# Kernel tuning notes

Measured on AMD Instinct MI355X. Metric: run time of the kernel, lower is better.

## Reference

```python
import jax, jax.numpy as jnp
import numpy as np

B, T, HID = 8, 1024, 1024
N_HEADS, HEAD = 16, HID // 16
MAX_F, BASE = 1024, 10000.0


def _rope_tables():
    inv_freq = 1.0 / (BASE ** (np.arange(0, HEAD, 2, dtype=np.float32) / HEAD))
    t = np.arange(MAX_F, dtype=np.float32)
    freqs = np.einsum('i,j->ij', t, inv_freq)  # (MAX_F, HEAD/2)
    emb = np.concatenate([freqs, freqs], axis=-1)  # (MAX_F, HEAD)
    return jnp.asarray(np.cos(emb)), jnp.asarray(np.sin(emb))


def setup_inputs() -> dict:
    key = jax.random.key(0)
    ks = jax.random.split(key, 6)
    x = jax.random.normal(ks[0], (B, T, HID), dtype=jnp.float32)
    Wq = jax.random.normal(ks[1], (HID, HID), dtype=jnp.float32) * 0.02
    Wk = jax.random.normal(ks[2], (HID, HID), dtype=jnp.float32) * 0.02
    Wv = jax.random.normal(ks[3], (HID, HID), dtype=jnp.float32) * 0.02
    Wo = jax.random.normal(ks[4], (HID, HID), dtype=jnp.float32) * 0.02
    cos, sin = _rope_tables()
    attn_mask = jnp.ones((B, T, T), dtype=jnp.int32)
    timestamp = jax.random.randint(ks[5], (B, T), 0, MAX_F, dtype=jnp.int32)
    return {"x": x, "Wq": Wq, "Wk": Wk, "Wv": Wv, "Wo": Wo,
            "cos": cos, "sin": sin, "attn_mask": attn_mask, "timestamp": timestamp}


def _rotate_half(u):
    u1, u2 = u[..., : HEAD // 2], u[..., HEAD // 2:]
    return jnp.concatenate([-u2, u1], axis=-1)


def reference(x, Wq, Wk, Wv, Wo, cos, sin, attn_mask, timestamp):
    Bx, Tx, _ = x.shape
    # QKV projections (nn.Linear: x @ W.T), reshape to (B, H, T, head)
    def proj(W):
        return (x @ W.T).reshape(Bx, Tx, N_HEADS, HEAD).transpose(0, 2, 1, 3)
    q, k, v = proj(Wq), proj(Wk), proj(Wv)
    # RoPE: gather cos/sin by timestamp, broadcast over heads (unsqueeze dim 1)
    c = cos[timestamp][:, None]  # (B, 1, T, head)
    s = sin[timestamp][:, None]
    q = q * c + _rotate_half(q) * s
    k = k * c + _rotate_half(k) * s
    # Masked SDPA
    scale = 1.0 / jnp.sqrt(jnp.float32(HEAD))
    scores = jnp.einsum('bhqd,bhkd->bhqk', q, k) * scale
    mask = attn_mask[:, None].astype(bool)  # (B, 1, T, T) broadcasts over heads
    scores = jnp.where(mask, scores, jnp.finfo(scores.dtype).min)
    attn = jax.nn.softmax(scores, axis=-1)
    out = jnp.einsum('bhqk,bhkd->bhqd', attn, v)
    out = out.transpose(0, 2, 1, 3).reshape(Bx, Tx, HID)
    return out @ Wo.T
```

## Files before the change

### kernel.cpp

```cpp
#include <hip/hip_runtime.h>
#include <hip/hip_bf16.h>

#define B_   8
#define T_   1024
#define HID_ 1024
#define NH_  16
#define HD_  64
#define K2   2048

typedef __attribute__((ext_vector_type(8))) short bf16x8;
typedef __attribute__((ext_vector_type(4))) float f32x4;

__device__ __forceinline__ void gl_lds16(const void* g, void* l) {
    __builtin_amdgcn_global_load_lds((const __attribute__((address_space(1))) void*)g,
                                     (__attribute__((address_space(3))) void*)l, 16, 0, 0);
}

__device__ __forceinline__ float fast_exp2(float x) {
    return __builtin_amdgcn_exp2f(x);
}

__global__ __launch_bounds__(256) void cast_bf16(const float* __restrict__ X,
                                                 __hip_bfloat16* __restrict__ Y) {
    int gid = blockIdx.x * 256 + threadIdx.x;
    int f = gid << 2;
    float4 xv = *(const float4*)(X + f);
    union { __hip_bfloat16 b[4]; ushort4 u; } p;
    p.b[0] = __float2bfloat16(xv.x);
    p.b[1] = __float2bfloat16(xv.y);
    p.b[2] = __float2bfloat16(xv.z);
    p.b[3] = __float2bfloat16(xv.w);
    *(ushort4*)(Y + f) = p.u;
}

__global__ __launch_bounds__(256) void dup_bf16_w(const float* __restrict__ X,
                                                  __hip_bfloat16* __restrict__ Y) {
    int gid = blockIdx.x * 256 + threadIdx.x;
    int f = gid << 2;
    int m = f >> 10, kk = f & 1023;
    float4 xv = *(const float4*)(X + f);
    union { __hip_bfloat16 b[4]; ushort4 u; } ph;
    ph.b[0] = __float2bfloat16(xv.x);
    ph.b[1] = __float2bfloat16(xv.y);
    ph.b[2] = __float2bfloat16(xv.z);
    ph.b[3] = __float2bfloat16(xv.w);
    size_t base = (size_t)m * K2 + kk;
    *(ushort4*)(Y + base) = ph.u;
    *(ushort4*)(Y + base + 1024) = ph.u;
}

__global__ __launch_bounds__(256) void mask_pack(const int* __restrict__ mask,
                                                 unsigned long long* __restrict__ mbits) {
    int gid = blockIdx.x * 256 + threadIdx.x;
    int wid = gid >> 6;
    int lane = threadIdx.x & 63;
    int m = mask[(size_t)wid * 64 + lane];
    unsigned long long bal = __ballot(m != 0);
    if (lane == 0) mbits[wid] = bal;
}

__global__ __launch_bounds__(256) void mask_dense(const unsigned long long* __restrict__ mbits,
                                                  unsigned int* __restrict__ tdense) {
    int gid = blockIdx.x * 256 + threadIdx.x;
    int e = gid >> 6;
    int lane = threadIdx.x & 63;
    int b = e >> 8, qt = (e >> 4) & 15, kt = e & 15;
    unsigned long long val = mbits[((size_t)(b * T_ + qt * 64 + lane)) * 16 + kt];
    unsigned long long bal = __ballot(val == ~0ull);
    if (lane == 0) tdense[e] = (bal == ~0ull) ? 1u : 0u;
}

template<int MODE, int KD>
__global__ __launch_bounds__(256, 4) void gemm_mfma(const __hip_bfloat16* __restrict__ A,
                                                    const __hip_bfloat16* __restrict__ Wp,
                                                    float* __restrict__ C0,
                                                    __hip_bfloat16* __restrict__ qbf,
                                                    __hip_bfloat16* __restrict__ kbf,
                                                    __hip_bfloat16* __restrict__ vt,
                                                    const float* __restrict__ cost,
                                                    const float* __restrict__ sint,
                                                    const int* __restrict__ ts) {
    __shared__ __hip_bfloat16 As[2][128 * 32];
    __shared__ __hip_bfloat16 Bs[2][128 * 32];
    const int tid = threadIdx.x;
    const int lane = tid & 63;
    const int w = tid >> 6;
    const int wm = w >> 1, wn = w & 1;
    const int m0 = blockIdx.y * 128, n0 = blockIdx.x * 128;
    const int r0 = tid >> 2;
    const int ks = (tid & 3) << 3;
    const int ml = lane & 15;
    const int kg = (lane >> 4) << 3;
    const int q4 = (lane >> 4) << 2;

    f32x4 acc[4][4];
#pragma unroll
    for (int i = 0; i < 4; ++i)
#pragma unroll
        for (int j = 0; j < 4; ++j) acc[i][j] = (f32x4){0.f, 0.f, 0.f, 0.f};

    for (int k0 = 0; k0 < KD; k0 += 64) {
#pragma unroll
        for (int c = 0; c < 2; ++c) {
            const int kc = k0 + c * 32 + ks;
            gl_lds16(A  + (size_t)(m0 + r0)      * KD + kc, &As[c][r0 * 32 + ks]);
            gl_lds16(A  + (size_t)(m0 + 64 + r0) * KD + kc, &As[c][(64 + r0) * 32 + ks]);
            gl_lds16(Wp + (size_t)(n0 + r0)      * KD + kc, &Bs[c][r0 * 32 + ks]);
            gl_lds16(Wp + (size_t)(n0 + 64 + r0) * KD + kc, &Bs[c][(64 + r0) * 32 + ks]);
        }
        __syncthreads();

#pragma unroll
        for (int c = 0; c < 2; ++c) {
            bf16x8 a[4], b[4];
#pragma unroll
            for (int mi = 0; mi < 4; ++mi)
                a[mi] = *(const bf16x8*)(&As[c][(wm * 64 + mi * 16 + ml) * 32 + kg]);
#pragma unroll
            for (int ni = 0; ni < 4; ++ni)
                b[ni] = *(const bf16x8*)(&Bs[c][(wn * 64 + ni * 16 + ml) * 32 + kg]);
#pragma unroll
            for (int mi = 0; mi < 4; ++mi)
#pragma unroll
                for (int ni = 0; ni < 4; ++ni)
                    acc[mi][ni] = __builtin_amdgcn_mfma_f32_16x16x32_bf16(a[mi], b[ni], acc[mi][ni], 0, 0, 0);
        }
        __syncthreads();
    }

    if (MODE == 0) {
#pragma unroll
        for (int mi = 0; mi < 4; ++mi)
#pragma unroll
            for (int ni = 0; ni < 4; ++ni) {
                int n = n0 + wn * 64 + ni * 16 + ml;
#pragma unroll
                for (int r = 0; r < 4; ++r) {
                    int m = m0 + wm * 64 + mi * 16 + q4 + r;
                    C0[(size_t)m * 1024 + n] = acc[mi][ni][r];
                }
            }
    } else {
        const int nB = n0 + wn * 64;
        const int sel = nB >> 10;
        const int h = (nB & 1023) >> 6;
        if (sel < 2) {
            __hip_bfloat16* dst = sel ? kbf : qbf;
#pragma unroll
            for (int mi = 0; mi < 4; ++mi) {
#pragma unroll
                for (int r = 0; r < 4; ++r) {
                    int m = m0 + wm * 64 + mi * 16 + q4 + r;
                    int tsv = ts[m];
                    int bb = m >> 10, t = m & 1023;
                    size_t rowoff = ((size_t)(bb * NH_ + h) * T_ + t) * HD_;
#pragma unroll
                    for (int ni = 0; ni < 4; ++ni) {
                        int d = ni * 16 + ml;
                        float c = cost[tsv * HD_ + d];
                        float s = sint[tsv * HD_ + d];
                        float u  = acc[mi][ni][r];
                        float up = acc[mi][ni ^ 2][r];
                        float o = (ni < 2) ? (u * c - up * s) : (u * c + up * s);
                        dst[rowoff + d] = __float2bfloat16(o);
                    }
                }
            }
        } else {
#pragma unroll
            for (int mi = 0; mi < 4; ++mi)
#pragma unroll
                for (int r = 0; r < 4; ++r) {
                    int m = m0 + wm * 64 + mi * 16 + q4 + r;
                    int bb = m >> 10, t = m & 1023;
#pragma unroll
                    for (int ni = 0; ni < 4; ++ni) {
                        int d = ni * 16 + ml;
                        vt[((size_t)(bb * NH_ + h) * HD_ + d) * T_ + t] =
                            __float2bfloat16(acc[mi][ni][r]);
                    }
                }
        }
    }
}

__global__ __launch_bounds__(256, 4) void flash_mfma(const __hip_bfloat16* __restrict__ qg,
                                                     const __hip_bfloat16* __restrict__ kg_,
                                                     const __hip_bfloat16* __restrict__ vtg,
                                                     const unsigned long long* __restrict__ mbits,
                                                     const unsigned int* __restrict__ tdense,
                                                     __hip_bfloat16* __restrict__ xs) {
    __shared__ __hip_bfloat16 Ks[2][64 * 64];
    __shared__ __hip_bfloat16 Vt[2][64 * 64];
    __shared__ __hip_bfloat16 Ps[4][16 * 64];
    const int id = blockIdx.x;
    const int qt = (id >> 3) & 15;
    const int hb = ((id >> 7) << 3) | (id & 7);
    const int h = hb & 15, b = hb >> 4;
    const int tid = threadIdx.x;
    const int lane = tid & 63;
    const int w = tid >> 6;
    const int ml = lane & 15;
    const int g4 = lane >> 4;
    const int kg8 = g4 << 3;
    const int q4 = g4 << 2;
    const int q0 = qt * 64;
    const size_t bh_off = (size_t)(b * NH_ + h) * T_ * HD_;
    const __hip_bfloat16* qb = qg + bh_off;
    const __hip_bfloat16* kb = kg_ + bh_off;
    const __hip_bfloat16* vtb = vtg + bh_off;
    const float SCL = 0.125f * 1.44269504f;

    const int srow = lane >> 3;
    const int sg8 = ((lane & 7) ^ srow) << 3;
    const int sx = ((g4 ^ (ml & 7)) << 4);
    const int pswz = (ml & 7) << 4;

    bf16x8 qf0 = *(const bf16x8*)(qb + (size_t)(q0 + w * 16 + ml) * HD_ + kg8);
    bf16x8 qf1 = *(const bf16x8*)(qb + (size_t)(q0 + w * 16 + ml) * HD_ + 32 + kg8);

    f32x4 acc_o[4];
    float lsum = 0.f;
#pragma unroll
    for (int i = 0; i < 4; ++i) acc_o[i] = (f32x4){0.f, 0.f, 0.f, 0.f};
    char* psw = (char*)&Ps[w][0];

#pragma unroll
    for (int p = 0; p < 2; ++p) {
        const int rbase = p * 32 + w * 8;
        gl_lds16(kb  + (size_t)(rbase + srow) * HD_ + sg8, &Ks[0][rbase * 64]);
        gl_lds16(vtb + (size_t)(rbase + srow) * T_  + sg8, &Vt[0][rbase * 64]);
    }

    for (int kt = 0; kt < 16; ++kt) {
        const int cur = kt & 1;
        __syncthreads();
        if (kt < 15) {
            const int k0n = (kt + 1) * 64;
            const int nb = cur ^ 1;
#pragma unroll
            for (int p = 0; p < 2; ++p) {
                const int rbase = p * 32 + w * 8;
                gl_lds16(kb  + (size_t)(k0n + rbase + srow) * HD_ + sg8, &Ks[nb][rbase * 64]);
                gl_lds16(vtb + (size_t)(rbase + srow) * T_ + k0n + sg8, &Vt[nb][rbase * 64]);
            }
        }

        f32x4 sacc[4];
#pragma unroll
        for (int ni = 0; ni < 4; ++ni) sacc[ni] = (f32x4){0.f, 0.f, 0.f, 0.f};
        const char* ksb = (const char*)&Ks[cur][0];
#pragma unroll
        for (int ni = 0; ni < 4; ++ni) {
            const char* rp = ksb + (ni * 16 + ml) * 128;
            bf16x8 kf0 = *(const bf16x8*)(rp + sx);
            bf16x8 kf1 = *(const bf16x8*)(rp + (sx ^ 64));
            sacc[ni] = __builtin_amdgcn_mfma_f32_16x16x32_bf16(kf0, qf0, sacc[ni], 0, 0, 0);
            sacc[ni] = __builtin_amdgcn_mfma_f32_16x16x32_bf16(kf1, qf1, sacc[ni], 0, 0, 0);
        }

        if (tdense[(b * 16 + qt) * 16 + kt]) {
#pragma unroll
            for (int ni = 0; ni < 4; ++ni) {
                float pv[4];
#pragma unroll
                for (int r = 0; r < 4; ++r) pv[r] = fast_exp2(sacc[ni][r] * SCL);
                lsum += (pv[0] + pv[1]) + (pv[2] + pv[3]);
                union { __hip_bfloat16 bb[4]; unsigned long long u8; } pk;
                pk.bb[0] = __float2bfloat16(pv[0]);
                pk.bb[1] = __float2bfloat16(pv[1]);
                pk.bb[2] = __float2bfloat16(pv[2]);
                pk.bb[3] = __float2bfloat16(pv[3]);
                *(unsigned long long*)(psw + ml * 128 + ((ni * 32 + g4 * 8) ^ pswz)) = pk.u8;
            }
        } else {
            unsigned long long mb =
                mbits[((size_t)(b * T_ + q0 + w * 16 + ml)) * 16 + kt];
#pragma unroll
            for (int ni = 0; ni < 4; ++ni) {
                float pv[4];
#pragma unroll
                for (int r = 0; r < 4; ++r) {
                    int kv = ni * 16 + q4 + r;
                    pv[r] = ((mb >> kv) & 1ull) ? fast_exp2(sacc[ni][r] * SCL) : 0.f;
                }
                lsum += (pv[0] + pv[1]) + (pv[2] + pv[3]);
                union { __hip_bfloat16 bb[4]; unsigned long long u8; } pk;
                pk.bb[0] = __float2bfloat16(pv[0]);
                pk.bb[1] = __float2bfloat16(pv[1]);
                pk.bb[2] = __float2bfloat16(pv[2]);
                pk.bb[3] = __float2bfloat16(pv[3]);
                *(unsigned long long*)(psw + ml * 128 + ((ni * 32 + g4 * 8) ^ pswz)) = pk.u8;
            }
        }

        bf16x8 pf0 = *(const bf16x8*)(psw + ml * 128 + sx);
        bf16x8 pf1 = *(const bf16x8*)(psw + ml * 128 + (sx ^ 64));

        const char* vsb = (const char*)&Vt[cur][0];
#pragma unroll
        for (int dt = 0; dt < 4; ++dt) {
            const char* rp = vsb + (dt * 16 + ml) * 128;
            bf16x8 vf0 = *(const bf16x8*)(rp + sx);
            bf16x8 vf1 = *(const bf16x8*)(rp + (sx ^ 64));
            acc_o[dt] = __builtin_amdgcn_mfma_f32_16x16x32_bf16(pf0, vf0, acc_o[dt], 0, 0, 0);
            acc_o[dt] = __builtin_amdgcn_mfma_f32_16x16x32_bf16(pf1, vf1, acc_o[dt], 0, 0, 0);
        }
    }

    float l = lsum;
    l += __shfl_xor(l, 16);
    l += __shfl_xor(l, 32);
#pragma unroll
    for (int r = 0; r < 4; ++r) {
        float lr = __shfl(l, q4 + r, 16);
        float inv = 1.0f / lr;
        size_t rb = (size_t)(b * T_ + q0 + w * 16 + q4 + r) * K2;
#pragma unroll
        for (int dt = 0; dt < 4; ++dt) {
            float val = acc_o[dt][r] * inv;
            int col = h * HD_ + dt * 16 + ml;
            __hip_bfloat16 hi = __float2bfloat16(val);
            __hip_bfloat16 lo = __float2bfloat16(val - __bfloat162float(hi));
            xs[rb + col] = hi;
            xs[rb + 1024 + col] = lo;
        }
    }
}

extern "C" void kernel_launch(void* const* d_in, const int* in_sizes, int n_in,
                              void* d_out, int out_size, void* d_ws, size_t ws_size,
                              hipStream_t stream) {
    const float* x    = (const float*)d_in[0];
    const float* Wq   = (const float*)d_in[1];
    const float* Wk   = (const float*)d_in[2];
    const float* Wv   = (const float*)d_in[3];
    const float* Wo   = (const float*)d_in[4];
    const float* cost = (const float*)d_in[5];
    const float* sint = (const float*)d_in[6];
    const int*   mask = (const int*)d_in[7];
    const int*   ts   = (const int*)d_in[8];
    float* out = (float*)d_out;

    const size_t MB = 1ull << 20;
    char* wsp = (char*)d_ws;
    __hip_bfloat16* qbf  = (__hip_bfloat16*)(wsp + 0 * MB);
    __hip_bfloat16* kbf  = (__hip_bfloat16*)(wsp + 16 * MB);
    __hip_bfloat16* vt   = (__hip_bfloat16*)(wsp + 32 * MB);
    __hip_bfloat16* xs   = (__hip_bfloat16*)(wsp + 48 * MB);
    __hip_bfloat16* xb   = (__hip_bfloat16*)(wsp + 80 * MB);
    __hip_bfloat16* wqkv = (__hip_bfloat16*)(wsp + 96 * MB);
    __hip_bfloat16* wo   = (__hip_bfloat16*)(wsp + 102 * MB);
    unsigned long long* mbits = (unsigned long long*)(wsp + 106 * MB);
    unsigned int* tdense = (unsigned int*)(wsp + 107 * MB);

    cast_bf16<<<8192, 256, 0, stream>>>(x, xb);
    cast_bf16<<<1024, 256, 0, stream>>>(Wq, wqkv);
    cast_bf16<<<1024, 256, 0, stream>>>(Wk, wqkv + (size_t)1024 * 1024);
    cast_bf16<<<1024, 256, 0, stream>>>(Wv, wqkv + (size_t)2048 * 1024);
    dup_bf16_w<<<1024, 256, 0, stream>>>(Wo, wo);
    mask_pack<<<32768, 256, 0, stream>>>(mask, mbits);
    mask_dense<<<512, 256, 0, stream>>>(mbits, tdense);

    gemm_mfma<2, 1024><<<dim3(24, 64), 256, 0, stream>>>(xb, wqkv, nullptr,
                                                         qbf, kbf, vt, cost, sint, ts);

    flash_mfma<<<2048, 256, 0, stream>>>(qbf, kbf, vt, mbits, tdense, xs);

    gemm_mfma<0, K2><<<dim3(8, 64), 256, 0, stream>>>(xs, wo, out,
                                                      nullptr, nullptr, nullptr,
                                                      nullptr, nullptr, nullptr);
}
```

Baseline: 318.0 us.

## Process 128 query rows per flash block to reuse K/V tiles across two groups

The flash attention kernel now has each wave handle two 16-row query groups, so each block covers 128 queries instead of 64 and the grid is halved. Every K and V tile staged in LDS is reused by twice as many MFMA operations, which halves the K/V global traffic and the per-tile sync overhead. The cost is more accumulator registers per thread and fewer blocks to spread across CUs. The GEMM launch bound is also raised to 5 waves per SIMD, which limits registers more tightly to allow higher occupancy.

```diff
diff --git a/kernel.cpp b/kernel.cpp
--- a/kernel.cpp
+++ b/kernel.cpp
@@ -71,7 +71,7 @@
 }
 
 template<int MODE, int KD>
-__global__ __launch_bounds__(256, 4) void gemm_mfma(const __hip_bfloat16* __restrict__ A,
+__global__ __launch_bounds__(256, 5) void gemm_mfma(const __hip_bfloat16* __restrict__ A,
                                                     const __hip_bfloat16* __restrict__ Wp,
                                                     float* __restrict__ C0,
                                                     __hip_bfloat16* __restrict__ qbf,
@@ -194,8 +194,8 @@
     __shared__ __hip_bfloat16 Vt[2][64 * 64];
     __shared__ __hip_bfloat16 Ps[4][16 * 64];
     const int id = blockIdx.x;
-    const int qt = (id >> 3) & 15;
-    const int hb = ((id >> 7) << 3) | (id & 7);
+    const int qt = (id >> 3) & 7;
+    const int hb = ((id >> 6) << 3) | (id & 7);
     const int h = hb & 15, b = hb >> 4;
     const int tid = threadIdx.x;
     const int lane = tid & 63;
@@ -204,7 +204,8 @@
     const int g4 = lane >> 4;
     const int kg8 = g4 << 3;
     const int q4 = g4 << 2;
-    const int q0 = qt * 64;
+    const int q0 = qt * 128;
+    const int qw = q0 + w * 32;
     const size_t bh_off = (size_t)(b * NH_ + h) * T_ * HD_;
     const __hip_bfloat16* qb = qg + bh_off;
     const __hip_bfloat16* kb = kg_ + bh_off;
@@ -215,14 +216,21 @@
     const int sg8 = ((lane & 7) ^ srow) << 3;
     const int sx = ((g4 ^ (ml & 7)) << 4);
     const int pswz = (ml & 7) << 4;
-
-    bf16x8 qf0 = *(const bf16x8*)(qb + (size_t)(q0 + w * 16 + ml) * HD_ + kg8);
-    bf16x8 qf1 = *(const bf16x8*)(qb + (size_t)(q0 + w * 16 + ml) * HD_ + 32 + kg8);
-
-    f32x4 acc_o[4];
-    float lsum = 0.f;
-#pragma unroll
-    for (int i = 0; i < 4; ++i) acc_o[i] = (f32x4){0.f, 0.f, 0.f, 0.f};
+    const int tdbase = (b * 16 + qt * 2 + (w >> 1)) * 16;
+
+    bf16x8 qf[2][2];
+#pragma unroll
+    for (int g = 0; g < 2; ++g) {
+        qf[g][0] = *(const bf16x8*)(qb + (size_t)(qw + g * 16 + ml) * HD_ + kg8);
+        qf[g][1] = *(const bf16x8*)(qb + (size_t)(qw + g * 16 + ml) * HD_ + 32 + kg8);
+    }
+
+    f32x4 acc_o[2][4];
+    float lsum[2] = {0.f, 0.f};
+#pragma unroll
+    for (int g = 0; g < 2; ++g)
+#pragma unroll
+        for (int i = 0; i < 4; ++i) acc_o[g][i] = (f32x4){0.f, 0.f, 0.f, 0.f};
     char* psw = (char*)&Ps[w][0];
 
 #pragma unroll
@@ -246,84 +254,96 @@
             }
         }
 
-        f32x4 sacc[4];
-#pragma unroll
-        for (int ni = 0; ni < 4; ++ni) sacc[ni] = (f32x4){0.f, 0.f, 0.f, 0.f};
+        f32x4 sacc[2][4];
+#pragma unroll
+        for (int g = 0; g < 2; ++g)
+#pragma unroll
+            for (int ni = 0; ni < 4; ++ni) sacc[g][ni] = (f32x4){0.f, 0.f, 0.f, 0.f};
         const char* ksb = (const char*)&Ks[cur][0];
 #pragma unroll
         for (int ni = 0; ni < 4; ++ni) {
             const char* rp = ksb + (ni * 16 + ml) * 128;
             bf16x8 kf0 = *(const bf16x8*)(rp + sx);
             bf16x8 kf1 = *(const bf16x8*)(rp + (sx ^ 64));
-            sacc[ni] = __builtin_amdgcn_mfma_f32_16x16x32_bf16(kf0, qf0, sacc[ni], 0, 0, 0);
-            sacc[ni] = __builtin_amdgcn_mfma_f32_16x16x32_bf16(kf1, qf1, sacc[ni], 0, 0, 0);
-        }
-
-        if (tdense[(b * 16 + qt) * 16 + kt]) {
-#pragma unroll
-            for (int ni = 0; ni < 4; ++ni) {
-                float pv[4];
-#pragma unroll
-                for (int r = 0; r < 4; ++r) pv[r] = fast_exp2(sacc[ni][r] * SCL);
-                lsum += (pv[0] + pv[1]) + (pv[2] + pv[3]);
-                union { __hip_bfloat16 bb[4]; unsigned long long u8; } pk;
-                pk.bb[0] = __float2bfloat16(pv[0]);
-                pk.bb[1] = __float2bfloat16(pv[1]);
-                pk.bb[2] = __float2bfloat16(pv[2]);
-                pk.bb[3] = __float2bfloat16(pv[3]);
-                *(unsigned long long*)(psw + ml * 128 + ((ni * 32 + g4 * 8) ^ pswz)) = pk.u8;
-            }
-        } else {
-            unsigned long long mb =
-                mbits[((size_t)(b * T_ + q0 + w * 16 + ml)) * 16 + kt];
-#pragma unroll
-            for (int ni = 0; ni < 4; ++ni) {
-                float pv[4];
-#pragma unroll
-                for (int r = 0; r < 4; ++r) {
-                    int kv = ni * 16 + q4 + r;
-                    pv[r] = ((mb >> kv) & 1ull) ? fast_exp2(sacc[ni][r] * SCL) : 0.f;
-                }
-                lsum += (pv[0] + pv[1]) + (pv[2] + pv[3]);
-                union { __hip_bfloat16 bb[4]; unsigned long long u8; } pk;
-                pk.bb[0] = __float2bfloat16(pv[0]);
-                pk.bb[1] = __float2bfloat16(pv[1]);
-                pk.bb[2] = __float2bfloat16(pv[2]);
-                pk.bb[3] = __float2bfloat16(pv[3]);
-                *(unsigned long long*)(psw + ml * 128 + ((ni * 32 + g4 * 8) ^ pswz)) = pk.u8;
-            }
-        }
-
-        bf16x8 pf0 = *(const bf16x8*)(psw + ml * 128 + sx);
-        bf16x8 pf1 = *(const bf16x8*)(psw + ml * 128 + (sx ^ 64));
-
+            sacc[0][ni] = __builtin_amdgcn_mfma_f32_16x16x32_bf16(kf0, qf[0][0], sacc[0][ni], 0, 0, 0);
+            sacc[0][ni] = __builtin_amdgcn_mfma_f32_16x16x32_bf16(kf1, qf[0][1], sacc[0][ni], 0, 0, 0);
+            sacc[1][ni] = __builtin_amdgcn_mfma_f32_16x16x32_bf16(kf0, qf[1][0], sacc[1][ni], 0, 0, 0);
+            sacc[1][ni] = __builtin_amdgcn_mfma_f32_16x16x32_bf16(kf1, qf[1][1], sacc[1][ni], 0, 0, 0);
+        }
+
+        const int dense = tdense[tdbase + kt];
         const char* vsb = (const char*)&Vt[cur][0];
-#pragma unroll
-        for (int dt = 0; dt < 4; ++dt) {
-            const char* rp = vsb + (dt * 16 + ml) * 128;
-            bf16x8 vf0 = *(const bf16x8*)(rp + sx);
-            bf16x8 vf1 = *(const bf16x8*)(rp + (sx ^ 64));
-            acc_o[dt] = __builtin_amdgcn_mfma_f32_16x16x32_bf16(pf0, vf0, acc_o[dt], 0, 0, 0);
-            acc_o[dt] = __builtin_amdgcn_mfma_f32_16x16x32_bf16(pf1, vf1, acc_o[dt], 0, 0, 0);
-        }
-    }
-
-    float l = lsum;
-    l += __shfl_xor(l, 16);
-    l += __shfl_xor(l, 32);
-#pragma unroll
-    for (int r = 0; r < 4; ++r) {
-        float lr = __shfl(l, q4 + r, 16);
-        float inv = 1.0f / lr;
-        size_t rb = (size_t)(b * T_ + q0 + w * 16 + q4 + r) * K2;
-#pragma unroll
-        for (int dt = 0; dt < 4; ++dt) {
-            float val = acc_o[dt][r] * inv;
-            int col = h * HD_ + dt * 16 + ml;
-            __hip_bfloat16 hi = __float2bfloat16(val);
-            __hip_bfloat16 lo = __float2bfloat16(val - __bfloat162float(hi));
-            xs[rb + col] = hi;
-            xs[rb + 1024 + col] = lo;
+
+#pragma unroll
+        for (int g = 0; g < 2; ++g) {
+            if (dense) {
+#pragma unroll
+                for (int ni = 0; ni < 4; ++ni) {
+                    float pv[4];
+#pragma unroll
+                    for (int r = 0; r < 4; ++r) pv[r] = fast_exp2(sacc[g][ni][r] * SCL);
+                    lsum[g] += (pv[0] + pv[1]) + (pv[2] + pv[3]);
+                    union { __hip_bfloat16 bb[4]; unsigned long long u8; } pk;
+                    pk.bb[0] = __float2bfloat16(pv[0]);
+                    pk.bb[1] = __float2bfloat16(pv[1]);
+                    pk.bb[2] = __float2bfloat16(pv[2]);
+                    pk.bb[3] = __float2bfloat16(pv[3]);
+                    *(unsigned long long*)(psw + ml * 128 + ((ni * 32 + g4 * 8) ^ pswz)) = pk.u8;
+                }
+            } else {
+                unsigned long long mb =
+                    mbits[((size_t)(b * T_ + qw + g * 16 + ml)) * 16 + kt];
+#pragma unroll
+                for (int ni = 0; ni < 4; ++ni) {
+                    float pv[4];
+#pragma unroll
+                    for (int r = 0; r < 4; ++r) {
+                        int kv = ni * 16 + q4 + r;
+                        pv[r] = ((mb >> kv) & 1ull) ? fast_exp2(sacc[g][ni][r] * SCL) : 0.f;
+                    }
+                    lsum[g] += (pv[0] + pv[1]) + (pv[2] + pv[3]);
+                    union { __hip_bfloat16 bb[4]; unsigned long long u8; } pk;
+                    pk.bb[0] = __float2bfloat16(pv[0]);
+                    pk.bb[1] = __float2bfloat16(pv[1]);
+                    pk.bb[2] = __float2bfloat16(pv[2]);
+                    pk.bb[3] = __float2bfloat16(pv[3]);
+                    *(unsigned long long*)(psw + ml * 128 + ((ni * 32 + g4 * 8) ^ pswz)) = pk.u8;
+                }
+            }
+
+            bf16x8 pf0 = *(const bf16x8*)(psw + ml * 128 + sx);
+            bf16x8 pf1 = *(const bf16x8*)(psw + ml * 128 + (sx ^ 64));
+
+#pragma unroll
+            for (int dt = 0; dt < 4; ++dt) {
+                const char* rp = vsb + (dt * 16 + ml) * 128;
+                bf16x8 vf0 = *(const bf16x8*)(rp + sx);
+                bf16x8 vf1 = *(const bf16x8*)(rp + (sx ^ 64));
+                acc_o[g][dt] = __builtin_amdgcn_mfma_f32_16x16x32_bf16(pf0, vf0, acc_o[g][dt], 0, 0, 0);
+                acc_o[g][dt] = __builtin_amdgcn_mfma_f32_16x16x32_bf16(pf1, vf1, acc_o[g][dt], 0, 0, 0);
+            }
+        }
+    }
+
+#pragma unroll
+    for (int g = 0; g < 2; ++g) {
+        float l = lsum[g];
+        l += __shfl_xor(l, 16);
+        l += __shfl_xor(l, 32);
+#pragma unroll
+        for (int r = 0; r < 4; ++r) {
+            float lr = __shfl(l, q4 + r, 16);
+            float inv = 1.0f / lr;
+            size_t rb = (size_t)(b * T_ + qw + g * 16 + q4 + r) * K2;
+#pragma unroll
+            for (int dt = 0; dt < 4; ++dt) {
+                float val = acc_o[g][dt][r] * inv;
+                int col = h * HD_ + dt * 16 + ml;
+                __hip_bfloat16 hi = __float2bfloat16(val);
+                __hip_bfloat16 lo = __float2bfloat16(val - __bfloat162float(hi));
+                xs[rb + col] = hi;
+                xs[rb + 1024 + col] = lo;
+            }
         }
     }
 }
@@ -365,7 +385,7 @@
     gemm_mfma<2, 1024><<<dim3(24, 64), 256, 0, stream>>>(xb, wqkv, nullptr,
                                                          qbf, kbf, vt, cost, sint, ts);
 
-    flash_mfma<<<2048, 256, 0, stream>>>(qbf, kbf, vt, mbits, tdense, xs);
+    flash_mfma<<<1024, 256, 0, stream>>>(qbf, kbf, vt, mbits, tdense, xs);
 
     gemm_mfma<0, K2><<<dim3(8, 64), 256, 0, stream>>>(xs, wo, out,
                                                       nullptr, nullptr, nullptr,
```

After: 456.6 us. 43.6% more time.
